# Kernel optimization log

Hardware: AMD Instinct MI355X
Metric: run time of the kernel (lower is better)

## Reference

```python
import jax, jax.numpy as jnp
import numpy as np

NB, NSITES, N_NGB, DIM, NG = 32, 65536, 13, 3, 48


def setup_inputs() -> dict:
    key = jax.random.key(0)
    k1, k2, k3, k4, k5 = jax.random.split(key, 5)
    In = jax.random.normal(k1, (NB, 1, NSITES), dtype=jnp.float32)
    # wtVC ~ Normal(mean=1.0, std=0.1), size (dim, N_ngb)
    wtVC = 1.0 + 0.1 * jax.random.normal(k2, (DIM, N_NGB), dtype=jnp.float32)
    # gdiags: (Ng*dim, Ng*dim) symmetry-rotation mixing matrix
    gdiags = jax.random.normal(k3, (NG * DIM, NG * DIM), dtype=jnp.float32)
    GnnPerms = jax.random.randint(k4, (NG, N_NGB), 0, N_NGB)
    NNsites = jax.random.randint(k5, (N_NGB, NSITES), 0, NSITES)
    return {"In": In, "wtVC": wtVC, "gdiags": gdiags,
            "GnnPerms": GnnPerms, "NNsites": NNsites}


def reference(In, wtVC, gdiags, GnnPerms, NNsites):
    Ng = GnnPerms.shape[0]
    dim, n_ngb = wtVC.shape
    # RotateParams: row g*dim+d of the permuted weight is wtVC[d, GnnPerms[g]]
    Wp = wtVC[:, GnnPerms]                              # [dim, Ng, N_ngb]
    Wp = jnp.transpose(Wp, (1, 0, 2)).reshape(Ng * dim, n_ngb)
    Wt = gdiags @ Wp                                    # [Ng*dim, N_ngb]
    # Final op in torch is sum over g / Ng; fold that into the weight to
    # avoid materializing the [Nb, Ng*dim, Nsites] intermediate.
    Wmean = Wt.reshape(Ng, dim, n_ngb).mean(axis=0)     # [dim, N_ngb]
    # RearrangeInput: gathered[b, j, s] = In[b, 0, NNsites[j, s]]
    gathered = In[:, 0, :][:, NNsites]                  # [Nb, N_ngb, Nsites]
    # out[b, d, s] = sum_j Wmean[d, j] * gathered[b, j, s]
    return jnp.einsum('dj,bjs->bds', Wmean, gathered)   # [Nb, dim, Nsites]
```

## Files before the change

### kernel.cpp

```cpp
#include <hip/hip_runtime.h>

#define NB_     32
#define NSITES_ 65536
#define NNGB_   13
#define DIM_    3
#define NG_     48
#define GD_     (NG_ * DIM_)

typedef unsigned uvec4_t __attribute__((ext_vector_type(4)));
typedef int      ivec4_t __attribute__((ext_vector_type(4)));

__global__ __launch_bounds__(256) void prep_kernel_78486(
    const float* __restrict__ In,
    const float* __restrict__ wtVC,
    const float* __restrict__ gdiags,
    const int*   __restrict__ perms,
    const int*   __restrict__ nn,
    float*  __restrict__ wm,
    ushort* __restrict__ InT,
    int nTransBlocks)
{
    const int t = threadIdx.x;
    if ((int)blockIdx.x < nTransBlocks) {
        const int tb = blockIdx.x;
        const int s0 = tb * 64;

        int keep = 0;
        if (t < NNGB_ * 16) {
            const int j = t >> 4, i4 = t & 15;
            ivec4_t v = *(const ivec4_t*)(nn + j * NSITES_ + s0 + 4 * i4);
            keep = v.x ^ v.y ^ v.z ^ v.w;
        }

        __shared__ ushort tile[64][40];
        const int sl = t & 63, bq = t >> 6;
#pragma unroll
        for (int r = 0; r < 8; r++) {
            int b = bq * 8 + r;
            float v = In[b * NSITES_ + s0 + sl];
            unsigned fu = __float_as_uint(v);
            fu = fu + 0x7FFFu + ((fu >> 16) & 1u);
            tile[sl][b] = (ushort)(fu >> 16);
        }
        __syncthreads();
        const int site = t >> 2, q = t & 3;
        uvec4_t val = *(const uvec4_t*)&tile[site][q * 8];
        __builtin_nontemporal_store(
            val, (uvec4_t*)(InT + (size_t)(s0 + site) * NB_ + q * 8));
        asm volatile("" :: "v"(keep));
    } else {
        const int p = blockIdx.x - nTransBlocks;
        const int d = p / NNGB_, j = p - NNGB_ * d;
        __shared__ float wpj[GD_];
        __shared__ float red[4];
        if (t < GD_) {
            int g = t / DIM_, dp = t - DIM_ * g;
            wpj[t] = wtVC[dp * NNGB_ + perms[g * NNGB_ + j]];
        }
        __syncthreads();
        float acc = 0.f;
        for (int e = t; e < NG_ * GD_; e += 256) {
            int g = e / GD_;
            int k = e - g * GD_;
            acc += gdiags[(g * DIM_ + d) * GD_ + k] * wpj[k];
        }
#pragma unroll
        for (int off = 32; off > 0; off >>= 1) acc += __shfl_down(acc, off, 64);
        if ((t & 63) == 0) red[t >> 6] = acc;
        __syncthreads();
        if (t == 0) wm[p] = (red[0] + red[1] + red[2] + red[3]) * (1.0f / NG_);
    }
}

__global__ __launch_bounds__(256) void gather_kernel_78486(
    const ushort* __restrict__ InT,
    const int*    __restrict__ nn,
    const float*  __restrict__ wm,
    float* __restrict__ out)
{
    const int t = blockIdx.x * 256 + threadIdx.x;
    const int q = t & 3;
    const int s = t >> 2;

    int idx[NNGB_];
#pragma unroll
    for (int j = 0; j < NNGB_; j++) idx[j] = nn[j * NSITES_ + s];

    uvec4_t u[NNGB_];
#pragma unroll
    for (int j = 0; j < NNGB_; j++)
        u[j] = *(const uvec4_t*)(InT + ((size_t)idx[j] << 5) + (q << 3));

    float a0[8], a1[8], a2[8];
#pragma unroll
    for (int i = 0; i < 8; i++) { a0[i] = 0.f; a1[i] = 0.f; a2[i] = 0.f; }

#pragma unroll
    for (int j = 0; j < NNGB_; j++) {
        unsigned uu[4] = {u[j].x, u[j].y, u[j].z, u[j].w};
        float v[8];
#pragma unroll
        for (int k = 0; k < 4; k++) {
            v[2 * k]     = __uint_as_float(uu[k] << 16);
            v[2 * k + 1] = __uint_as_float(uu[k] & 0xFFFF0000u);
        }
        float w0 = wm[j], w1 = wm[NNGB_ + j], w2 = wm[2 * NNGB_ + j];
#pragma unroll
        for (int i = 0; i < 8; i++) {
            a0[i] += w0 * v[i];
            a1[i] += w1 * v[i];
            a2[i] += w2 * v[i];
        }
    }

#pragma unroll
    for (int i = 0; i < 8; i++) {
        int b = q * 8 + i;
        size_t base = (size_t)b * DIM_ * NSITES_ + s;
        out[base]               = a0[i];
        out[base + NSITES_]     = a1[i];
        out[base + 2 * NSITES_] = a2[i];
    }
}

__global__ __launch_bounds__(256) void gather_fallback_78486(
    const float* __restrict__ In,
    const int*   __restrict__ nn,
    const float* __restrict__ wm,
    float* __restrict__ out)
{
    const int t = blockIdx.x * 256 + threadIdx.x;
    const int s = t & (NSITES_ - 1);
    const int b = t >> 16;
    float x0 = 0.f, x1 = 0.f, x2 = 0.f;
#pragma unroll
    for (int j = 0; j < NNGB_; j++) {
        int idx = nn[j * NSITES_ + s];
        float v = In[b * NSITES_ + idx];
        x0 += wm[0 * NNGB_ + j] * v;
        x1 += wm[1 * NNGB_ + j] * v;
        x2 += wm[2 * NNGB_ + j] * v;
    }
    out[(b * DIM_ + 0) * NSITES_ + s] = x0;
    out[(b * DIM_ + 1) * NSITES_ + s] = x1;
    out[(b * DIM_ + 2) * NSITES_ + s] = x2;
}

extern "C" void kernel_launch(void* const* d_in, const int* in_sizes, int n_in,
                              void* d_out, int out_size, void* d_ws, size_t ws_size,
                              hipStream_t stream)
{
    const float* In     = (const float*)d_in[0];
    const float* wtVC   = (const float*)d_in[1];
    const float* gdiags = (const float*)d_in[2];
    const int*   perms  = (const int*)d_in[3];
    const int*   nn     = (const int*)d_in[4];
    float* out = (float*)d_out;

    float*  wm  = (float*)d_ws;
    ushort* InT = (ushort*)((char*)d_ws + 1024);

    const size_t need = 1024 + (size_t)NSITES_ * NB_ * sizeof(ushort);
    const int nTrans = NSITES_ / 64;

    if (ws_size >= need) {
        prep_kernel_78486<<<nTrans + DIM_ * NNGB_, 256, 0, stream>>>(
            In, wtVC, gdiags, perms, nn, wm, InT, nTrans);
        gather_kernel_78486<<<(NSITES_ * 4) / 256, 256, 0, stream>>>(
            InT, nn, wm, out);
    } else {
        prep_kernel_78486<<<DIM_ * NNGB_, 256, 0, stream>>>(
            In, wtVC, gdiags, perms, nn, wm, (ushort*)nullptr, 0);
        gather_fallback_78486<<<(NSITES_ * NB_) / 256, 256, 0, stream>>>(
            In, nn, wm, out);
    }
}
```

Before: 92.95 us.

## Split transposed bf16 input into two batch-half tables with separate gather passes

The transposed bf16 input table is split into two 2 MB tables, each holding 16 batches per site, and the gather runs as two launches, one per half. Each gather table is half the size, so the random neighbour reads have a smaller footprint that fits L2/MALL cache better. The cost is an extra kernel launch, nn indices read twice, and each thread now covers only half a site's batches, so more threads load the same indices.

```diff
diff --git a/kernel.cpp b/kernel.cpp
--- a/kernel.cpp
+++ b/kernel.cpp
@@ -17,7 +17,8 @@
     const int*   __restrict__ perms,
     const int*   __restrict__ nn,
     float*  __restrict__ wm,
-    ushort* __restrict__ InT,
+    ushort* __restrict__ InTA,
+    ushort* __restrict__ InTB,
     int nTransBlocks)
 {
     const int t = threadIdx.x;
@@ -45,8 +46,9 @@
         __syncthreads();
         const int site = t >> 2, q = t & 3;
         uvec4_t val = *(const uvec4_t*)&tile[site][q * 8];
+        ushort* T = (q < 2) ? InTA : InTB;
         __builtin_nontemporal_store(
-            val, (uvec4_t*)(InT + (size_t)(s0 + site) * NB_ + q * 8));
+            val, (uvec4_t*)(T + ((size_t)(s0 + site) << 4) + ((q & 1) << 3)));
         asm volatile("" :: "v"(keep));
     } else {
         const int p = blockIdx.x - nTransBlocks;
@@ -72,15 +74,16 @@
     }
 }
 
-__global__ __launch_bounds__(256) void gather_kernel_78486(
-    const ushort* __restrict__ InT,
+__global__ __launch_bounds__(256) void gather_half_78486(
+    const ushort* __restrict__ T,
     const int*    __restrict__ nn,
     const float*  __restrict__ wm,
-    float* __restrict__ out)
+    float* __restrict__ out,
+    int bBase)
 {
     const int t = blockIdx.x * 256 + threadIdx.x;
-    const int q = t & 3;
-    const int s = t >> 2;
+    const int h = t & 1;
+    const int s = t >> 1;
 
     int idx[NNGB_];
 #pragma unroll
@@ -89,7 +92,7 @@
     uvec4_t u[NNGB_];
 #pragma unroll
     for (int j = 0; j < NNGB_; j++)
-        u[j] = *(const uvec4_t*)(InT + ((size_t)idx[j] << 5) + (q << 3));
+        u[j] = *(const uvec4_t*)(T + ((size_t)idx[j] << 4) + (h << 3));
 
     float a0[8], a1[8], a2[8];
 #pragma unroll
@@ -115,7 +118,7 @@
 
 #pragma unroll
     for (int i = 0; i < 8; i++) {
-        int b = q * 8 + i;
+        int b = bBase + h * 8 + i;
         size_t base = (size_t)b * DIM_ * NSITES_ + s;
         out[base]               = a0[i];
         out[base + NSITES_]     = a1[i];
@@ -157,20 +160,25 @@
     const int*   nn     = (const int*)d_in[4];
     float* out = (float*)d_out;
 
-    float*  wm  = (float*)d_ws;
-    ushort* InT = (ushort*)((char*)d_ws + 1024);
+    float*  wm   = (float*)d_ws;
+    ushort* InTA = (ushort*)((char*)d_ws + 1024);
+    ushort* InTB = (ushort*)((char*)d_ws + 1024 +
+                             (size_t)NSITES_ * 16 * sizeof(ushort));
 
     const size_t need = 1024 + (size_t)NSITES_ * NB_ * sizeof(ushort);
     const int nTrans = NSITES_ / 64;
 
     if (ws_size >= need) {
         prep_kernel_78486<<<nTrans + DIM_ * NNGB_, 256, 0, stream>>>(
-            In, wtVC, gdiags, perms, nn, wm, InT, nTrans);
-        gather_kernel_78486<<<(NSITES_ * 4) / 256, 256, 0, stream>>>(
-            InT, nn, wm, out);
+            In, wtVC, gdiags, perms, nn, wm, InTA, InTB, nTrans);
+        gather_half_78486<<<(NSITES_ * 2) / 256, 256, 0, stream>>>(
+            InTA, nn, wm, out, 0);
+        gather_half_78486<<<(NSITES_ * 2) / 256, 256, 0, stream>>>(
+            InTB, nn, wm, out, 16);
     } else {
         prep_kernel_78486<<<DIM_ * NNGB_, 256, 0, stream>>>(
-            In, wtVC, gdiags, perms, nn, wm, (ushort*)nullptr, 0);
+            In, wtVC, gdiags, perms, nn, wm, (ushort*)nullptr,
+            (ushort*)nullptr, 0);
         gather_fallback_78486<<<(NSITES_ * NB_) / 256, 256, 0, stream>>>(
             In, nn, wm, out);
     }
```

Result: slower. 98.75 us (+6.2%).
